# Kernel optimization log

Measured on AMD Instinct MI355X. Metric: run time of the kernel, lower is better.

Reference implementation:

```python
import jax, jax.numpy as jnp
import numpy as np

B, R, C, O, I = 256, 1152, 10, 16, 8  # batch, num_routes, num_capsules, out_ch, in_ch
NUM_ITERS = 3


def setup_inputs() -> dict:
    key = jax.random.key(0)
    kx, kw = jax.random.split(key)
    x = jax.random.normal(kx, (B, R, I), dtype=jnp.float32)
    W = jax.random.normal(kw, (R, C, O, I), dtype=jnp.float32)
    return {"x": x, "W": W}


def _squash_elementwise(s):
    # Faithful to the original: squared_norm is summed over the LAST dim of
    # s_j, which has size 1 in the torch code, so squash acts elementwise:
    # v = s^2 * s / ((1 + s^2) * sqrt(s^2))
    sq = s * s
    return sq * s / ((1.0 + sq) * jnp.sqrt(sq))


def reference(x, W):
    # u_hat[b,r,c,o] = W[r,c,o,:] @ x[b,r,:]
    u_hat = jnp.einsum('rcoi,bri->brco', W, x)  # (B,R,C,O)
    b_ij = jnp.zeros((R, C), dtype=x.dtype)
    v = None
    for it in range(NUM_ITERS):
        # legacy F.softmax default on 4D (1,R,C,1) is dim=1 -> over routes
        c_ij = jax.nn.softmax(b_ij, axis=0)               # (R,C)
        s_j = jnp.einsum('rc,brco->bco', c_ij, u_hat)     # (B,C,O)
        v = _squash_elementwise(s_j)                      # (B,C,O)
        if it < NUM_ITERS - 1:
            # agreement: <u_hat, v> over out dim, averaged over batch
            a_ij = jnp.einsum('brco,bco->brc', u_hat, v)  # (B,R,C)
            b_ij = b_ij + a_ij.mean(axis=0)
    return v[..., None]  # (B,C,O,1) matching v_j.squeeze(1)
```

## Files before the change

### kernel.cpp

```cpp
#include <hip/hip_runtime.h>
#include <math.h>


#define B_ 256
#define R_ 1152
#define N_ 160
#define K_ 9216
#define NS 128
#define KB 72
#define LDK 104
#define LDB 136

#define PART_ELEMS ((size_t)B_*NS*N_)
#define BIJ_BOFF   (PART_ELEMS*2)
#define VT_BOFF    (BIJ_BOFF + (size_t)R_*10*4)

typedef __attribute__((ext_vector_type(8))) short short8;
typedef __attribute__((ext_vector_type(4))) float f32x4;

static __device__ __forceinline__ short f2bf(float f) {
    unsigned u = __float_as_uint(f);
    unsigned r = (u + 0x7fffu + ((u >> 16) & 1u)) >> 16;
    return (short)r;
}

__global__ __launch_bounds__(256) void k_gemm(const float* __restrict__ X,
                                              const float* __restrict__ W,
                                              float* __restrict__ bij,
                                              _Float16* __restrict__ part,
                                              int it) {
    __shared__ short As[128 * LDK];
    __shared__ short Bs[160 * LDK];
    __shared__ float cs[90];
    __shared__ float red[40];
    __shared__ float dsm[10];
    const int tid = threadIdx.x;
    const int ks = blockIdx.x >> 1, bt = blockIdx.x & 1;
    const int b0 = bt * 128, k0 = ks * KB, r0 = ks * 9;

    if (it == 0) {
        if (tid < 90) cs[tid] = 1.0f / 1152.0f;
        if (bt == 0 && tid < 90) bij[r0 * 10 + tid] = 0.0f;
    } else {
        float dcol[10];
        #pragma unroll
        for (int c = 0; c < 10; ++c) dcol[c] = 0.0f;
        for (int r = tid; r < R_; r += 256) {
            #pragma unroll
            for (int c = 0; c < 10; ++c) dcol[c] += __expf(bij[r * 10 + c]);
        }
        const int lane = tid & 63, wv = tid >> 6;
        #pragma unroll
        for (int c = 0; c < 10; ++c) {
            float s = dcol[c];
            #pragma unroll
            for (int off = 32; off > 0; off >>= 1) s += __shfl_down(s, off);
            if (lane == 0) red[wv * 10 + c] = s;
        }
        __syncthreads();
        if (tid < 10)
            dsm[tid] = red[tid] + red[10 + tid] + red[20 + tid] + red[30 + tid];
        __syncthreads();
        if (tid < 90) {
            int rr = tid / 10, cc = tid - rr * 10;
            cs[tid] = __expf(bij[(r0 + rr) * 10 + cc]) / dsm[cc];
        }
    }

    #pragma unroll
    for (int j = 0; j < 9; ++j) {
        int q = j * 256 + tid;
        int bb = q / 18, kf = q - bb * 18;
        float4 a = *(const float4*)(X + (size_t)(b0 + bb) * K_ + k0 + kf * 4);
        short4 h = make_short4(f2bf(a.x), f2bf(a.y), f2bf(a.z), f2bf(a.w));
        *(short4*)(&As[bb * LDK + kf * 4]) = h;
    }
    #pragma unroll
    for (int j = 0; j < 3; ++j) {
        int q = j * 256 + tid;
        int bb = q / 6, ch = q - bb * 6;
        *(short4*)(&As[bb * LDK + 72 + ch * 4]) = make_short4(0, 0, 0, 0);
    }
    {
        const float* Wsl = W + (size_t)r0 * 1280;
        #pragma unroll
        for (int j = 0; j < 12; ++j) {
            int q = j * 256 + tid;
            if (q < 2880) {
                int rl = q / 320;
                int rem = q - rl * 320;
                int c = rem >> 5;
                int o = (rem & 31) >> 1;
                int i4 = rem & 1;
                float4 w = *(const float4*)(Wsl + (size_t)q * 4);
                float sc = cs[rl * 10 + c];
                int nn = c * 16 + o;
                int kk = rl * 8 + i4 * 4;
                short4 h = make_short4(f2bf(w.x * sc), f2bf(w.y * sc),
                                       f2bf(w.z * sc), f2bf(w.w * sc));
                *(short4*)(&Bs[nn * LDK + kk]) = h;
            }
        }
        #pragma unroll
        for (int j = 0; j < 4; ++j) {
            int q = j * 256 + tid;
            if (q < 960) {
                int nn = q / 6, ch = q - nn * 6;
                *(short4*)(&Bs[nn * LDK + 72 + ch * 4]) = make_short4(0, 0, 0, 0);
            }
        }
    }
    __syncthreads();

    const int wv = tid >> 6, lane = tid & 63;
    const int lrow = lane & 15, quad = lane >> 4;
    f32x4 acc[2][10];
    #pragma unroll
    for (int mi = 0; mi < 2; ++mi)
        #pragma unroll
        for (int nt = 0; nt < 10; ++nt) acc[mi][nt] = (f32x4)(0.0f);

    #pragma unroll
    for (int ksp = 0; ksp < 3; ++ksp) {
        const int ko = ksp * 32 + quad * 8;
        short8 afr[2], bfr[10];
        #pragma unroll
        for (int mi = 0; mi < 2; ++mi)
            afr[mi] = *(const short8*)(&As[((wv * 2 + mi) * 16 + lrow) * LDK + ko]);
        #pragma unroll
        for (int nt = 0; nt < 10; ++nt)
            bfr[nt] = *(const short8*)(&Bs[(nt * 16 + lrow) * LDK + ko]);
        #pragma unroll
        for (int mi = 0; mi < 2; ++mi)
            #pragma unroll
            for (int nt = 0; nt < 10; ++nt)
                acc[mi][nt] = __builtin_amdgcn_mfma_f32_16x16x32_bf16(
                    afr[mi], bfr[nt], acc[mi][nt], 0, 0, 0);
    }

    #pragma unroll
    for (int mi = 0; mi < 2; ++mi) {
        int bbase = b0 + (wv * 2 + mi) * 16 + quad * 4;
        #pragma unroll
        for (int reg = 0; reg < 4; ++reg) {
            _Float16* P = part + (size_t)(bbase + reg) * (NS * N_) + ks * N_ + lrow;
            #pragma unroll
            for (int nt = 0; nt < 10; ++nt)
                P[nt * 16] = (_Float16)acc[mi][nt][reg];
        }
    }
}

__global__ void k_reduce(const _Float16* __restrict__ part,
                         float* __restrict__ out,
                         short* __restrict__ vt, int fin) {
    const int n = threadIdx.x, b = blockIdx.x;
    if (n < 160) {
        const _Float16* p = part + (size_t)b * (NS * N_) + n;
        float s = 0.0f;
        #pragma unroll 8
        for (int ks = 0; ks < NS; ++ks) s += (float)p[ks * N_];
        float v = s * fabsf(s) / (1.0f + s * s);
        if (fin) out[b * N_ + n] = v;
        else     vt[n * 256 + b] = f2bf(v);
    }
}

__global__ __launch_bounds__(256) void k_gtdot(const float* __restrict__ X,
                                               const float* __restrict__ W,
                                               const short* __restrict__ Vt,
                                               float* __restrict__ bij) {
    __shared__ short SM2[32640];
    short* As = SM2;
    short* Bs = SM2 + 80 * LDB;
    float* LG = (float*)SM2;
    const int tid = threadIdx.x;
    const int kt = blockIdx.x >> 1, bh = blockIdx.x & 1;
    const int k0 = kt * 72, r0 = kt * 9, b0 = bh * 128;

    #pragma unroll
    for (int j = 0; j < 9; ++j) {
        int q = j * 256 + tid;
        int bb = q / 18, kf = q - bb * 18;
        float4 a = *(const float4*)(X + (size_t)(b0 + bb) * K_ + k0 + kf * 4);
        As[(kf * 4 + 0) * LDB + bb] = f2bf(a.x);
        As[(kf * 4 + 1) * LDB + bb] = f2bf(a.y);
        As[(kf * 4 + 2) * LDB + bb] = f2bf(a.z);
        As[(kf * 4 + 3) * LDB + bb] = f2bf(a.w);
    }
    #pragma unroll
    for (int j = 0; j < 10; ++j) {
        int q = j * 256 + tid;
        int n = q >> 4, s = q & 15;
        *(short8*)(&Bs[n * LDB + s * 8]) =
            *(const short8*)(Vt + n * 256 + b0 + s * 8);
    }
    __syncthreads();

    const int wv = tid >> 6, lane = tid & 63;
    const int lrow = lane & 15, quad = lane >> 4;
    f32x4 acc[5][3];
    #pragma unroll
    for (int mt = 0; mt < 5; ++mt)
        #pragma unroll
        for (int sl = 0; sl < 3; ++sl) acc[mt][sl] = (f32x4)(0.0f);

    #pragma unroll
    for (int kb = 0; kb < 4; ++kb) {
        const int ko = kb * 32 + quad * 8;
        short8 af[5], bf[3];
        #pragma unroll
        for (int mt = 0; mt < 5; ++mt)
            af[mt] = *(const short8*)(&As[(mt * 16 + lrow) * LDB + ko]);
        #pragma unroll
        for (int sl = 0; sl < 3; ++sl) {
            int nt = wv + sl * 4;
            if (nt < 10)
                bf[sl] = *(const short8*)(&Bs[(nt * 16 + lrow) * LDB + ko]);
        }
        #pragma unroll
        for (int mt = 0; mt < 5; ++mt)
            #pragma unroll
            for (int sl = 0; sl < 3; ++sl)
                if (wv + sl * 4 < 10)
                    acc[mt][sl] = __builtin_amdgcn_mfma_f32_16x16x32_bf16(
                        af[mt], bf[sl], acc[mt][sl], 0, 0, 0);
    }
    __syncthreads();

    #pragma unroll
    for (int mt = 0; mt < 5; ++mt) {
        #pragma unroll
        for (int sl = 0; sl < 3; ++sl) {
            int nt = wv + sl * 4;
            if (nt < 10) {
                #pragma unroll
                for (int reg = 0; reg < 4; ++reg) {
                    int m = mt * 16 + quad * 4 + reg;
                    if (m < 72)
                        LG[m * 165 + nt * 16 + lrow] = acc[mt][sl][reg];
                }
            }
        }
    }
    __syncthreads();
    if (tid < 90) {
        int rl = tid / 10, c = tid - rl * 10;
        int r = r0 + rl;
        const float4* wp = (const float4*)(W + (size_t)r * 1280 + c * 128);
        float s = 0.0f;
        #pragma unroll
        for (int o = 0; o < 16; ++o) {
            float4 wa = wp[o * 2], wb = wp[o * 2 + 1];
            const float* g = &LG[(rl * 8) * 165 + c * 16 + o];
            s += wa.x * g[0]       + wa.y * g[165]     + wa.z * g[2 * 165] +
                 wa.w * g[3 * 165] + wb.x * g[4 * 165] + wb.y * g[5 * 165] +
                 wb.z * g[6 * 165] + wb.w * g[7 * 165];
        }
        atomicAdd(&bij[r * 10 + c], s * (1.0f / B_));
    }
}

extern "C" void kernel_launch(void* const* d_in, const int* in_sizes, int n_in,
                              void* d_out, int out_size, void* d_ws, size_t ws_size,
                              hipStream_t stream) {
    const float* x = (const float*)d_in[0];
    const float* W = (const float*)d_in[1];
    char* ws      = (char*)d_ws;
    _Float16* part = (_Float16*)ws;
    float* bij    = (float*)(ws + BIJ_BOFF);
    short* vt     = (short*)(ws + VT_BOFF);
    float* outf   = (float*)d_out;

    for (int it = 0; it < 3; ++it) {
        k_gemm<<<256, 256, 0, stream>>>(x, W, bij, part, it);
        k_reduce<<<256, 256, 0, stream>>>(part, outf, vt, it == 2);
        if (it < 2) k_gtdot<<<256, 256, 0, stream>>>(x, W, vt, bij);
    }
}
```

Before: 131.9 us.

## Fuse all routing iterations into one persistent kernel with grid barriers

```diff
diff --git a/kernel.cpp b/kernel.cpp
--- a/kernel.cpp
+++ b/kernel.cpp
@@ -14,6 +14,13 @@
 #define PART_ELEMS ((size_t)B_*NS*N_)
 #define BIJ_BOFF   (PART_ELEMS*2)
 #define VT_BOFF    (BIJ_BOFF + (size_t)R_*10*4)
+#define BAR_BOFF   (VT_BOFF + (size_t)N_*B_*2)
+#define BAR_BYTES  2048
+
+#define ASG_OFF    0
+#define WF_OFF     26624
+#define SCR_OFF    72704
+#define SMEM_BYTES 120224
 
 typedef __attribute__((ext_vector_type(8))) short short8;
 typedef __attribute__((ext_vector_type(4))) float f32x4;
@@ -24,48 +31,63 @@
     return (short)r;
 }
 
-__global__ __launch_bounds__(256) void k_gemm(const float* __restrict__ X,
+static __device__ __forceinline__ void st_u16_dev(void* p, unsigned v) {
+    asm volatile("global_store_short %0, %1, off sc1"
+                 :: "v"(p), "v"(v) : "memory");
+}
+static __device__ __forceinline__ void st_f32_dev(void* p, float v) {
+    asm volatile("global_store_dword %0, %1, off sc1"
+                 :: "v"(p), "v"(v) : "memory");
+}
+
+static __device__ __forceinline__ void gbar(unsigned* __restrict__ bar,
+                                            int id, int tid) {
+    __syncthreads();
+    if (tid == 0) {
+        unsigned* base = bar + id * 64;
+        unsigned xcd;
+        asm volatile("s_getreg_b32 %0, hwreg(HW_REG_XCC_ID)" : "=s"(xcd));
+        xcd &= 7;
+        bool lead = (__hip_atomic_fetch_add(base + xcd, 1u, __ATOMIC_RELAXED,
+                                            __HIP_MEMORY_SCOPE_AGENT) == 0u);
+        __hip_atomic_fetch_add(base + 8, 1u, __ATOMIC_RELAXED,
+                               __HIP_MEMORY_SCOPE_AGENT);
+        if (lead) {
+            __builtin_amdgcn_fence(__ATOMIC_ACQUIRE, "agent");
+            while (__hip_atomic_load(base + 8, __ATOMIC_RELAXED,
+                                     __HIP_MEMORY_SCOPE_AGENT) < 256u)
+                __builtin_amdgcn_s_sleep(1);
+            __hip_atomic_fetch_add(base + 16, 1u, __ATOMIC_RELAXED,
+                                   __HIP_MEMORY_SCOPE_AGENT);
+        }
+        while (__hip_atomic_load(base + 16, __ATOMIC_RELAXED,
+                                 __HIP_MEMORY_SCOPE_AGENT) < 8u)
+            __builtin_amdgcn_s_sleep(1);
+    }
+    __syncthreads();
+    __builtin_amdgcn_fence(__ATOMIC_ACQUIRE, "workgroup");
+}
+
+__global__ __launch_bounds__(256) void k_caps(const float* __restrict__ X,
                                               const float* __restrict__ W,
+                                              _Float16* __restrict__ part,
                                               float* __restrict__ bij,
-                                              _Float16* __restrict__ part,
-                                              int it) {
-    __shared__ short As[128 * LDK];
-    __shared__ short Bs[160 * LDK];
+                                              short* __restrict__ vt,
+                                              float* __restrict__ out,
+                                              unsigned* __restrict__ bar) {
+    __shared__ __align__(16) char smem[SMEM_BYTES];
+    short* Asg = (short*)(smem + ASG_OFF);
+    float* Wf  = (float*)(smem + WF_OFF);
+    short* Bs  = (short*)(smem + SCR_OFF);
+    short* Ast = (short*)(smem + SCR_OFF);
+    float* LG  = (float*)(smem + SCR_OFF);
     __shared__ float cs[90];
     __shared__ float red[40];
     __shared__ float dsm[10];
+
     const int tid = threadIdx.x;
     const int ks = blockIdx.x >> 1, bt = blockIdx.x & 1;
     const int b0 = bt * 128, k0 = ks * KB, r0 = ks * 9;
-
-    if (it == 0) {
-        if (tid < 90) cs[tid] = 1.0f / 1152.0f;
-        if (bt == 0 && tid < 90) bij[r0 * 10 + tid] = 0.0f;
-    } else {
-        float dcol[10];
-        #pragma unroll
-        for (int c = 0; c < 10; ++c) dcol[c] = 0.0f;
-        for (int r = tid; r < R_; r += 256) {
-            #pragma unroll
-            for (int c = 0; c < 10; ++c) dcol[c] += __expf(bij[r * 10 + c]);
-        }
-        const int lane = tid & 63, wv = tid >> 6;
-        #pragma unroll
-        for (int c = 0; c < 10; ++c) {
-            float s = dcol[c];
-            #pragma unroll
-            for (int off = 32; off > 0; off >>= 1) s += __shfl_down(s, off);
-            if (lane == 0) red[wv * 10 + c] = s;
-        }
-        __syncthreads();
-        if (tid < 10)
-            dsm[tid] = red[tid] + red[10 + tid] + red[20 + tid] + red[30 + tid];
-        __syncthreads();
-        if (tid < 90) {
-            int rr = tid / 10, cc = tid - rr * 10;
-            cs[tid] = __expf(bij[(r0 + rr) * 10 + cc]) / dsm[cc];
-        }
-    }
 
     #pragma unroll
     for (int j = 0; j < 9; ++j) {
@@ -73,13 +95,13 @@
         int bb = q / 18, kf = q - bb * 18;
         float4 a = *(const float4*)(X + (size_t)(b0 + bb) * K_ + k0 + kf * 4);
         short4 h = make_short4(f2bf(a.x), f2bf(a.y), f2bf(a.z), f2bf(a.w));
-        *(short4*)(&As[bb * LDK + kf * 4]) = h;
+        *(short4*)(&Asg[bb * LDK + kf * 4]) = h;
     }
     #pragma unroll
     for (int j = 0; j < 3; ++j) {
         int q = j * 256 + tid;
         int bb = q / 6, ch = q - bb * 6;
-        *(short4*)(&As[bb * LDK + 72 + ch * 4]) = make_short4(0, 0, 0, 0);
+        *(short4*)(&Asg[bb * LDK + 72 + ch * 4]) = make_short4(0, 0, 0, 0);
     }
     {
         const float* Wsl = W + (size_t)r0 * 1280;
@@ -93,12 +115,54 @@
                 int o = (rem & 31) >> 1;
                 int i4 = rem & 1;
                 float4 w = *(const float4*)(Wsl + (size_t)q * 4);
-                float sc = cs[rl * 10 + c];
-                int nn = c * 16 + o;
-                int kk = rl * 8 + i4 * 4;
+                *(float4*)(&Wf[(c * 16 + o) * 72 + rl * 8 + i4 * 4]) = w;
+            }
+        }
+    }
+    if (bt == 0 && tid < 90)
+        st_f32_dev(&bij[r0 * 10 + tid], 0.0f);
+
+    for (int it = 0; it < 3; ++it) {
+        if (it == 0) {
+            if (tid < 90) cs[tid] = 1.0f / 1152.0f;
+        } else {
+            float dcol[10];
+            #pragma unroll
+            for (int c = 0; c < 10; ++c) dcol[c] = 0.0f;
+            for (int r = tid; r < R_; r += 256) {
+                #pragma unroll
+                for (int c = 0; c < 10; ++c) dcol[c] += __expf(bij[r * 10 + c]);
+            }
+            const int lane = tid & 63, wv = tid >> 6;
+            #pragma unroll
+            for (int c = 0; c < 10; ++c) {
+                float s = dcol[c];
+                #pragma unroll
+                for (int off = 32; off > 0; off >>= 1) s += __shfl_down(s, off);
+                if (lane == 0) red[wv * 10 + c] = s;
+            }
+            __syncthreads();
+            if (tid < 10)
+                dsm[tid] = red[tid] + red[10 + tid] + red[20 + tid] + red[30 + tid];
+            __syncthreads();
+            if (tid < 90) {
+                int rr = tid / 10, cc = tid - rr * 10;
+                cs[tid] = __expf(bij[(r0 + rr) * 10 + cc]) / dsm[cc];
+            }
+        }
+        __syncthreads();
+
+        #pragma unroll
+        for (int j = 0; j < 12; ++j) {
+            int q = j * 256 + tid;
+            if (q < 2880) {
+                int nn = q / 18, kk4 = q - nn * 18;
+                float4 w = *(const float4*)(Wf + nn * 72 + kk4 * 4);
+                int rl = kk4 >> 1;
+                float sc = cs[rl * 10 + (nn >> 4)];
                 short4 h = make_short4(f2bf(w.x * sc), f2bf(w.y * sc),
                                        f2bf(w.z * sc), f2bf(w.w * sc));
-                *(short4*)(&Bs[nn * LDK + kk]) = h;
+                *(short4*)(&Bs[nn * LDK + kk4 * 4]) = h;
             }
         }
         #pragma unroll
@@ -109,155 +173,144 @@
                 *(short4*)(&Bs[nn * LDK + 72 + ch * 4]) = make_short4(0, 0, 0, 0);
             }
         }
-    }
-    __syncthreads();
-
-    const int wv = tid >> 6, lane = tid & 63;
-    const int lrow = lane & 15, quad = lane >> 4;
-    f32x4 acc[2][10];
-    #pragma unroll
-    for (int mi = 0; mi < 2; ++mi)
+        __syncthreads();
+
+        {
+            const int wv = tid >> 6, lane = tid & 63;
+            const int lrow = lane & 15, quad = lane >> 4;
+            f32x4 acc[2][10];
+            #pragma unroll
+            for (int mi = 0; mi < 2; ++mi)
+                #pragma unroll
+                for (int nt = 0; nt < 10; ++nt) acc[mi][nt] = (f32x4)(0.0f);
+
+            #pragma unroll
+            for (int ksp = 0; ksp < 3; ++ksp) {
+                const int ko = ksp * 32 + quad * 8;
+                short8 afr[2], bfr[10];
+                #pragma unroll
+                for (int mi = 0; mi < 2; ++mi)
+                    afr[mi] = *(const short8*)(&Asg[((wv * 2 + mi) * 16 + lrow) * LDK + ko]);
+                #pragma unroll
+                for (int nt = 0; nt < 10; ++nt)
+                    bfr[nt] = *(const short8*)(&Bs[(nt * 16 + lrow) * LDK + ko]);
+                #pragma unroll
+                for (int mi = 0; mi < 2; ++mi)
+                    #pragma unroll
+                    for (int nt = 0; nt < 10; ++nt)
+                        acc[mi][nt] = __builtin_amdgcn_mfma_f32_16x16x32_bf16(
+                            afr[mi], bfr[nt], acc[mi][nt], 0, 0, 0);
+            }
+            #pragma unroll
+            for (int mi = 0; mi < 2; ++mi) {
+                int bbase = b0 + (wv * 2 + mi) * 16 + quad * 4;
+                #pragma unroll
+                for (int reg = 0; reg < 4; ++reg) {
+                    _Float16* P = part + (size_t)(bbase + reg) * (NS * N_) + ks * N_ + lrow;
+                    #pragma unroll
+                    for (int nt = 0; nt < 10; ++nt) {
+                        _Float16 h = (_Float16)acc[mi][nt][reg];
+                        st_u16_dev((void*)(P + nt * 16),
+                                   (unsigned)__builtin_bit_cast(unsigned short, h));
+                    }
+                }
+            }
+        }
+        gbar(bar, it * 3 + 0, tid);
+
+        if (tid < 160) {
+            const int b = blockIdx.x;
+            const _Float16* p = part + (size_t)b * (NS * N_) + tid;
+            float s = 0.0f;
+            #pragma unroll 8
+            for (int kk = 0; kk < NS; ++kk) s += (float)p[kk * N_];
+            float v = s * fabsf(s) / (1.0f + s * s);
+            if (it == 2) out[b * N_ + tid] = v;
+            else st_u16_dev((void*)&vt[tid * 256 + b],
+                            (unsigned)(unsigned short)f2bf(v));
+        }
+        if (it == 2) break;
+        gbar(bar, it * 3 + 1, tid);
+
         #pragma unroll
-        for (int nt = 0; nt < 10; ++nt) acc[mi][nt] = (f32x4)(0.0f);
-
-    #pragma unroll
-    for (int ksp = 0; ksp < 3; ++ksp) {
-        const int ko = ksp * 32 + quad * 8;
-        short8 afr[2], bfr[10];
-        #pragma unroll
-        for (int mi = 0; mi < 2; ++mi)
-            afr[mi] = *(const short8*)(&As[((wv * 2 + mi) * 16 + lrow) * LDK + ko]);
-        #pragma unroll
-        for (int nt = 0; nt < 10; ++nt)
-            bfr[nt] = *(const short8*)(&Bs[(nt * 16 + lrow) * LDK + ko]);
-        #pragma unroll
-        for (int mi = 0; mi < 2; ++mi)
-            #pragma unroll
-            for (int nt = 0; nt < 10; ++nt)
-                acc[mi][nt] = __builtin_amdgcn_mfma_f32_16x16x32_bf16(
-                    afr[mi], bfr[nt], acc[mi][nt], 0, 0, 0);
-    }
-
-    #pragma unroll
-    for (int mi = 0; mi < 2; ++mi) {
-        int bbase = b0 + (wv * 2 + mi) * 16 + quad * 4;
-        #pragma unroll
-        for (int reg = 0; reg < 4; ++reg) {
-            _Float16* P = part + (size_t)(bbase + reg) * (NS * N_) + ks * N_ + lrow;
-            #pragma unroll
-            for (int nt = 0; nt < 10; ++nt)
-                P[nt * 16] = (_Float16)acc[mi][nt][reg];
-        }
-    }
-}
-
-__global__ void k_reduce(const _Float16* __restrict__ part,
-                         float* __restrict__ out,
-                         short* __restrict__ vt, int fin) {
-    const int n = threadIdx.x, b = blockIdx.x;
-    if (n < 160) {
-        const _Float16* p = part + (size_t)b * (NS * N_) + n;
-        float s = 0.0f;
-        #pragma unroll 8
-        for (int ks = 0; ks < NS; ++ks) s += (float)p[ks * N_];
-        float v = s * fabsf(s) / (1.0f + s * s);
-        if (fin) out[b * N_ + n] = v;
-        else     vt[n * 256 + b] = f2bf(v);
-    }
-}
-
-__global__ __launch_bounds__(256) void k_gtdot(const float* __restrict__ X,
-                                               const float* __restrict__ W,
-                                               const short* __restrict__ Vt,
-                                               float* __restrict__ bij) {
-    __shared__ short SM2[32640];
-    short* As = SM2;
-    short* Bs = SM2 + 80 * LDB;
-    float* LG = (float*)SM2;
-    const int tid = threadIdx.x;
-    const int kt = blockIdx.x >> 1, bh = blockIdx.x & 1;
-    const int k0 = kt * 72, r0 = kt * 9, b0 = bh * 128;
-
-    #pragma unroll
-    for (int j = 0; j < 9; ++j) {
-        int q = j * 256 + tid;
-        int bb = q / 18, kf = q - bb * 18;
-        float4 a = *(const float4*)(X + (size_t)(b0 + bb) * K_ + k0 + kf * 4);
-        As[(kf * 4 + 0) * LDB + bb] = f2bf(a.x);
-        As[(kf * 4 + 1) * LDB + bb] = f2bf(a.y);
-        As[(kf * 4 + 2) * LDB + bb] = f2bf(a.z);
-        As[(kf * 4 + 3) * LDB + bb] = f2bf(a.w);
-    }
-    #pragma unroll
-    for (int j = 0; j < 10; ++j) {
-        int q = j * 256 + tid;
-        int n = q >> 4, s = q & 15;
-        *(short8*)(&Bs[n * LDB + s * 8]) =
-            *(const short8*)(Vt + n * 256 + b0 + s * 8);
-    }
-    __syncthreads();
-
-    const int wv = tid >> 6, lane = tid & 63;
-    const int lrow = lane & 15, quad = lane >> 4;
-    f32x4 acc[5][3];
-    #pragma unroll
-    for (int mt = 0; mt < 5; ++mt)
-        #pragma unroll
-        for (int sl = 0; sl < 3; ++sl) acc[mt][sl] = (f32x4)(0.0f);
-
-    #pragma unroll
-    for (int kb = 0; kb < 4; ++kb) {
-        const int ko = kb * 32 + quad * 8;
-        short8 af[5], bf[3];
-        #pragma unroll
-        for (int mt = 0; mt < 5; ++mt)
-            af[mt] = *(const short8*)(&As[(mt * 16 + lrow) * LDB + ko]);
-        #pragma unroll
-        for (int sl = 0; sl < 3; ++sl) {
-            int nt = wv + sl * 4;
-            if (nt < 10)
-                bf[sl] = *(const short8*)(&Bs[(nt * 16 + lrow) * LDB + ko]);
-        }
-        #pragma unroll
-        for (int mt = 0; mt < 5; ++mt)
-            #pragma unroll
-            for (int sl = 0; sl < 3; ++sl)
-                if (wv + sl * 4 < 10)
-                    acc[mt][sl] = __builtin_amdgcn_mfma_f32_16x16x32_bf16(
-                        af[mt], bf[sl], acc[mt][sl], 0, 0, 0);
-    }
-    __syncthreads();
-
-    #pragma unroll
-    for (int mt = 0; mt < 5; ++mt) {
-        #pragma unroll
-        for (int sl = 0; sl < 3; ++sl) {
-            int nt = wv + sl * 4;
-            if (nt < 10) {
-                #pragma unroll
-                for (int reg = 0; reg < 4; ++reg) {
-                    int m = mt * 16 + quad * 4 + reg;
-                    if (m < 72)
-                        LG[m * 165 + nt * 16 + lrow] = acc[mt][sl][reg];
+        for (int j = 0; j < 9; ++j) {
+            int q = j * 256 + tid;
+            int bb = q / 18, kf = q - bb * 18;
+            short4 a = *(const short4*)(&Asg[bb * LDK + kf * 4]);
+            Ast[(kf * 4 + 0) * LDB + bb] = a.x;
+            Ast[(kf * 4 + 1) * LDB + bb] = a.y;
+            Ast[(kf * 4 + 2) * LDB + bb] = a.z;
+            Ast[(kf * 4 + 3) * LDB + bb] = a.w;
+        }
+        __syncthreads();
+
+        {
+            const int wv = tid >> 6, lane = tid & 63;
+            const int lrow = lane & 15, quad = lane >> 4;
+            f32x4 acc[5][3];
+            #pragma unroll
+            for (int mt = 0; mt < 5; ++mt)
+                #pragma unroll
+                for (int sl = 0; sl < 3; ++sl) acc[mt][sl] = (f32x4)(0.0f);
+
+            #pragma unroll
+            for (int kb = 0; kb < 4; ++kb) {
+                const int ko = kb * 32 + quad * 8;
+                short8 af[5], bf[3];
+                #pragma unroll
+                for (int mt = 0; mt < 5; ++mt)
+                    af[mt] = *(const short8*)(&Ast[(mt * 16 + lrow) * LDB + ko]);
+                #pragma unroll
+                for (int sl = 0; sl < 3; ++sl) {
+                    int nt = wv + sl * 4;
+                    if (nt < 10)
+                        bf[sl] = *(const short8*)(vt + (nt * 16 + lrow) * 256 + b0 + ko);
                 }
-            }
-        }
-    }
-    __syncthreads();
-    if (tid < 90) {
-        int rl = tid / 10, c = tid - rl * 10;
-        int r = r0 + rl;
-        const float4* wp = (const float4*)(W + (size_t)r * 1280 + c * 128);
-        float s = 0.0f;
-        #pragma unroll
-        for (int o = 0; o < 16; ++o) {
-            float4 wa = wp[o * 2], wb = wp[o * 2 + 1];
-            const float* g = &LG[(rl * 8) * 165 + c * 16 + o];
-            s += wa.x * g[0]       + wa.y * g[165]     + wa.z * g[2 * 165] +
-                 wa.w * g[3 * 165] + wb.x * g[4 * 165] + wb.y * g[5 * 165] +
-                 wb.z * g[6 * 165] + wb.w * g[7 * 165];
-        }
-        atomicAdd(&bij[r * 10 + c], s * (1.0f / B_));
+                #pragma unroll
+                for (int mt = 0; mt < 5; ++mt)
+                    #pragma unroll
+                    for (int sl = 0; sl < 3; ++sl)
+                        if (wv + sl * 4 < 10)
+                            acc[mt][sl] = __builtin_amdgcn_mfma_f32_16x16x32_bf16(
+                                af[mt], bf[sl], acc[mt][sl], 0, 0, 0);
+            }
+            __syncthreads();
+
+            #pragma unroll
+            for (int mt = 0; mt < 5; ++mt) {
+                #pragma unroll
+                for (int sl = 0; sl < 3; ++sl) {
+                    int nt = wv + sl * 4;
+                    if (nt < 10) {
+                        #pragma unroll
+                        for (int reg = 0; reg < 4; ++reg) {
+                            int m = mt * 16 + quad * 4 + reg;
+                            if (m < 72)
+                                LG[m * 165 + nt * 16 + lrow] = acc[mt][sl][reg];
+                        }
+                    }
+                }
+            }
+        }
+        __syncthreads();
+        if (tid < 90) {
+            int rl = tid / 10, c = tid - rl * 10;
+            int r = r0 + rl;
+            const float* wbase = Wf + (c * 16) * 72 + rl * 8;
+            float s = 0.0f;
+            #pragma unroll
+            for (int o = 0; o < 16; ++o) {
+                const float* wp = wbase + o * 72;
+                float4 wa = *(const float4*)(wp);
+                float4 wb = *(const float4*)(wp + 4);
+                const float* g = &LG[(rl * 8) * 165 + c * 16 + o];
+                s += wa.x * g[0]       + wa.y * g[165]     + wa.z * g[2 * 165] +
+                     wa.w * g[3 * 165] + wb.x * g[4 * 165] + wb.y * g[5 * 165] +
+                     wb.z * g[6 * 165] + wb.w * g[7 * 165];
+            }
+            atomicAdd(&bij[r * 10 + c], s * (1.0f / B_));
+        }
+        gbar(bar, it * 3 + 2, tid);
     }
 }
 
@@ -266,15 +319,14 @@
                               hipStream_t stream) {
     const float* x = (const float*)d_in[0];
     const float* W = (const float*)d_in[1];
-    char* ws      = (char*)d_ws;
+    char* ws       = (char*)d_ws;
     _Float16* part = (_Float16*)ws;
-    float* bij    = (float*)(ws + BIJ_BOFF);
-    short* vt     = (short*)(ws + VT_BOFF);
-    float* outf   = (float*)d_out;
-
-    for (int it = 0; it < 3; ++it) {
-        k_gemm<<<256, 256, 0, stream>>>(x, W, bij, part, it);
-        k_reduce<<<256, 256, 0, stream>>>(part, outf, vt, it == 2);
-        if (it < 2) k_gtdot<<<256, 256, 0, stream>>>(x, W, vt, bij);
-    }
-}
+    float* bij     = (float*)(ws + BIJ_BOFF);
+    short* vt      = (short*)(ws + VT_BOFF);
+    unsigned* bar  = (unsigned*)(ws + BAR_BOFF);
+    float* outf    = (float*)d_out;
+
+    hipMemsetAsync((void*)bar, 0, BAR_BYTES, stream);
+
+    k_caps<<<256, 256, 0, stream>>>(x, W, part, bij, vt, outf, bar);
+}
```

After: 296.5 us. 2.25x slower.
